# Kernel tuning notes

Measured on AMD Instinct MI355X. Metric: run time of the kernel, lower is better.

Reference implementation:

```python
import jax, jax.numpy as jnp
import numpy as np

EPS = 1e-8  # torch F.cosine_similarity default eps


def setup_inputs() -> dict:
    key = jax.random.key(0)
    k1, k2 = jax.random.split(key)
    B, D, C = 8192, 1024, 1000
    x = jax.random.normal(k1, (B, D), dtype=jnp.float32)
    W = jax.random.normal(k2, (D, C), dtype=jnp.float32) * 0.02
    b = jnp.zeros((C,), dtype=jnp.float32)
    return {"x": x, "W": W, "b": b}


def reference(x, W, b):
    B = x.shape[0]
    # classifier logits -> softmax probs
    logits = x @ W + b                              # [B, C]
    logp = jax.nn.log_softmax(logits, axis=1)       # [B, C]
    pred = jnp.exp(logp)
    # per-row sum of p * log p (negative entropy), matches pred*log(pred) loop
    loss = jnp.sum(pred * logp, axis=-1)            # [B]
    # per-row mean cosine similarity against all rows (incl. self)
    norms = jnp.maximum(jnp.linalg.norm(x, axis=1, keepdims=True), EPS)
    xn = x / norms                                  # [B, D]
    sim = xn @ xn.T                                 # [B, B]
    weight = jnp.sum(sim, axis=1) / B               # [B]
    return loss * weight
```

## Files before the change

kernel.cpp:

```cpp
#include <hip/hip_runtime.h>
#include <hip/hip_bf16.h>
#include <cstdint>
#include <cstddef>

typedef __attribute__((ext_vector_type(8))) short bf16x8;
typedef __attribute__((ext_vector_type(4))) float f32x4;

__device__ __forceinline__ unsigned short f2bf(float f) {
  union { float f; unsigned u; } v; v.f = f;
  unsigned r = v.u + 0x7FFFu + ((v.u >> 16) & 1u);
  return (unsigned short)(r >> 16);
}

__device__ __forceinline__ float bf2f(unsigned short h) {
  union { float f; unsigned u; } c; c.u = ((unsigned)h) << 16;
  return c.f;
}

__device__ __forceinline__ void gload_lds16(const void* g, void* l) {
  __builtin_amdgcn_global_load_lds(
      (const __attribute__((address_space(1))) unsigned int*)g,
      (__attribute__((address_space(3))) unsigned int*)l, 16, 0, 0);
}

__global__ __launch_bounds__(1024) void k01_prep(const float* __restrict__ W,
                                                 unsigned short* __restrict__ wtf,
                                                 const float* __restrict__ x,
                                                 unsigned short* __restrict__ xbf,
                                                 float* __restrict__ rnorm,
                                                 float* __restrict__ sp) {
  __shared__ __align__(16) char sm[83968];
  int tid = threadIdx.x;
  int b = blockIdx.x;
  int lane = tid & 63;
  int wid = tid >> 6;

  int k0 = (b & 15) * 64;
  int c0 = (b >> 4) * 64;
  int tx = tid & 63;
  int ty = tid >> 6;
  float wreg[4];
#pragma unroll
  for (int i = 0; i < 4; ++i) {
    int c = c0 + tx;
    wreg[i] = (c < 1000) ? W[(size_t)(k0 + i * 16 + ty) * 1000 + c] : 0.f;
  }

  {
    float (*sblk)[1024] = (float(*)[1024])sm;
    int row0 = b * 32 + wid * 2;
    const float4* xr0 = (const float4*)(x + (size_t)row0 * 1024);
    const float4* xr1 = (const float4*)(x + (size_t)(row0 + 1) * 1024);
    float4 v[2][4];
#pragma unroll
    for (int j = 0; j < 4; ++j) v[0][j] = xr0[lane + j * 64];
#pragma unroll
    for (int j = 0; j < 4; ++j) v[1][j] = xr1[lane + j * 64];
    float ss0 = 0.f, ss1 = 0.f;
#pragma unroll
    for (int j = 0; j < 4; ++j) {
      ss0 += v[0][j].x * v[0][j].x + v[0][j].y * v[0][j].y +
             v[0][j].z * v[0][j].z + v[0][j].w * v[0][j].w;
      ss1 += v[1][j].x * v[1][j].x + v[1][j].y * v[1][j].y +
             v[1][j].z * v[1][j].z + v[1][j].w * v[1][j].w;
    }
#pragma unroll
    for (int m = 1; m < 64; m <<= 1) {
      ss0 += __shfl_xor(ss0, m);
      ss1 += __shfl_xor(ss1, m);
    }
    float rn0 = 1.f / fmaxf(sqrtf(ss0), 1e-8f);
    float rn1 = 1.f / fmaxf(sqrtf(ss1), 1e-8f);
    if (lane == 0) {
      rnorm[row0] = rn0;
      rnorm[row0 + 1] = rn1;
    }
    float4 sacc[4];
#pragma unroll
    for (int j = 0; j < 4; ++j) {
      ushort4 h0, h1;
      h0.x = f2bf(v[0][j].x); h0.y = f2bf(v[0][j].y);
      h0.z = f2bf(v[0][j].z); h0.w = f2bf(v[0][j].w);
      h1.x = f2bf(v[1][j].x); h1.y = f2bf(v[1][j].y);
      h1.z = f2bf(v[1][j].z); h1.w = f2bf(v[1][j].w);
      ((ushort4*)(xbf + (size_t)row0 * 1024))[lane + j * 64] = h0;
      ((ushort4*)(xbf + (size_t)(row0 + 1) * 1024))[lane + j * 64] = h1;
      sacc[j].x = v[0][j].x * rn0 + v[1][j].x * rn1;
      sacc[j].y = v[0][j].y * rn0 + v[1][j].y * rn1;
      sacc[j].z = v[0][j].z * rn0 + v[1][j].z * rn1;
      sacc[j].w = v[0][j].w * rn0 + v[1][j].w * rn1;
    }
#pragma unroll
    for (int j = 0; j < 4; ++j) ((float4*)sblk[wid])[j * 64 + lane] = sacc[j];
    __syncthreads();
    float acc = 0.f;
#pragma unroll
    for (int w = 0; w < 16; ++w) acc += sblk[w][tid];
    sp[(size_t)b * 1024 + tid] = acc;
  }

  {
    float (*tile2)[72] = (float(*)[72])(sm + 65536);
#pragma unroll
    for (int i = 0; i < 4; ++i) tile2[tx][i * 16 + ty] = wreg[i];
    __syncthreads();
    if (tid < 512) {
      int fi = tid >> 6;
      int l = tid & 63;
      int cf = fi >> 1;
      int kf = fi & 1;
      int r2 = cf * 16 + (l & 15);
      int c2 = kf * 32 + (l >> 4) * 8;
      float4 va = *(const float4*)&tile2[r2][c2];
      float4 vb = *(const float4*)&tile2[r2][c2 + 4];
      uint4 o;
      o.x = (unsigned)f2bf(va.x) | ((unsigned)f2bf(va.y) << 16);
      o.y = (unsigned)f2bf(va.z) | ((unsigned)f2bf(va.w) << 16);
      o.z = (unsigned)f2bf(vb.x) | ((unsigned)f2bf(vb.y) << 16);
      o.w = (unsigned)f2bf(vb.z) | ((unsigned)f2bf(vb.w) << 16);
      size_t fg = (size_t)(c0 / 16 + cf) * 32 + (k0 / 32 + kf);
      *(uint4*)((char*)wtf + fg * 1024 + (size_t)l * 16) = o;
    }
  }
}

__global__ __launch_bounds__(256) void k2_sred(const float* __restrict__ sp,
                                               float* __restrict__ s) {
  __shared__ float red[4][64];
  int t = threadIdx.x;
  int dd = t & 63;
  int g = t >> 6;
  int d = blockIdx.x * 64 + dd;
  float acc = 0.f;
#pragma unroll 8
  for (int b = g * 64; b < g * 64 + 64; ++b) acc += sp[(size_t)b * 1024 + d];
  red[g][dd] = acc;
  __syncthreads();
  if (g == 0) s[d] = red[0][dd] + red[1][dd] + red[2][dd] + red[3][dd];
}

__global__ __launch_bounds__(256) void k3_gemm(const unsigned short* __restrict__ xbf,
                                               const unsigned short* __restrict__ wtf,
                                               const float* __restrict__ bias,
                                               float* __restrict__ pm,
                                               float* __restrict__ pz,
                                               float* __restrict__ ps) {
  __shared__ __align__(16) char lds[32768];

  int tid = threadIdx.x;
  int lane = tid & 63;
  int wid = tid >> 6;
  int wc = wid & 1;
  int wr = wid >> 1;
  int cb = blockIdx.x >> 6;
  int rb = blockIdx.x & 63;
  int C0 = cb * 128;
  int R0 = rb * 128;

  float bv[4][4];
#pragma unroll
  for (int mf = 0; mf < 4; ++mf)
#pragma unroll
    for (int q = 0; q < 4; ++q) {
      int cls_g = C0 + wc * 64 + mf * 16 + (lane >> 4) * 4 + q;
      bv[mf][q] = (cls_g < 1000) ? bias[cls_g] : -1e30f;
    }
  f32x4 acc[4][4];
#pragma unroll
  for (int mf = 0; mf < 4; ++mf)
#pragma unroll
    for (int nf = 0; nf < 4; ++nf)
#pragma unroll
      for (int q = 0; q < 4; ++q) acc[mf][nf][q] = bv[mf][q];

  const char* gB = (const char*)(xbf + (size_t)R0 * 1024);
  int grow = (tid >> 3) & 7;
  int gswz = ((tid & 7) ^ grow) << 4;

  auto stageB = [&](int kt, int bb) {
    char* lB = lds + bb * 16384;
#pragma unroll
    for (int i = 0; i < 4; ++i) {
      size_t row = i * 32 + (tid >> 3);
      gload_lds16(gB + row * 2048 + kt * 128 + gswz, lB + i * 4096 + tid * 16);
    }
  };

  const char* gAf = (const char*)wtf +
                    ((size_t)(cb * 8 + wc * 4) * 32) * 1024 + (size_t)lane * 16;

  int rsw = (lane & 7) << 4;
  int kcol = (lane >> 4) * 16;

  stageB(0, 0);
  __syncthreads();
  int cur = 0;
  for (int t = 0; t < 16; ++t) {
    if (t < 15) stageB(t + 1, cur ^ 1);
    bf16x8 a[4][2], bb[4][2];
#pragma unroll
    for (int mf = 0; mf < 4; ++mf)
#pragma unroll
      for (int ks = 0; ks < 2; ++ks)
        a[mf][ks] = *(const bf16x8*)(gAf + (size_t)(mf * 32 + t * 2 + ks) * 1024);
    const char* B = lds + cur * 16384;
#pragma unroll
    for (int nf = 0; nf < 4; ++nf)
#pragma unroll
      for (int ks = 0; ks < 2; ++ks)
        bb[nf][ks] = *(const bf16x8*)(B + (wr * 64 + nf * 16 + (lane & 15)) * 128 +
                                      ((ks * 64 + kcol) ^ rsw));
    __builtin_amdgcn_s_setprio(1);
#pragma unroll
    for (int ks = 0; ks < 2; ++ks)
#pragma unroll
      for (int mf = 0; mf < 4; ++mf)
#pragma unroll
        for (int nf = 0; nf < 4; ++nf)
          acc[mf][nf] = __builtin_amdgcn_mfma_f32_16x16x32_bf16(a[mf][ks], bb[nf][ks],
                                                                acc[mf][nf], 0, 0, 0);
    __builtin_amdgcn_s_setprio(0);
    __syncthreads();
    cur ^= 1;
  }

  float* mm = (float*)lds;
  float* zz = mm + 256;
  float* sv = zz + 256;
#pragma unroll
  for (int nf = 0; nf < 4; ++nf) {
    float m1 = -1e30f;
#pragma unroll
    for (int mf = 0; mf < 4; ++mf)
#pragma unroll
      for (int q = 0; q < 4; ++q) m1 = fmaxf(m1, acc[mf][nf][q]);
    m1 = fmaxf(m1, __shfl_xor(m1, 16));
    m1 = fmaxf(m1, __shfl_xor(m1, 32));
    float z1 = 0.f, s1 = 0.f;
#pragma unroll
    for (int mf = 0; mf < 4; ++mf)
#pragma unroll
      for (int q = 0; q < 4; ++q) {
        float tt = acc[mf][nf][q] - m1;
        float e = expf(tt);
        z1 += e;
        s1 += e * tt;
      }
    z1 += __shfl_xor(z1, 16); z1 += __shfl_xor(z1, 32);
    s1 += __shfl_xor(s1, 16); s1 += __shfl_xor(s1, 32);
    if (lane < 16) {
      int r = wr * 64 + nf * 16 + lane;
      mm[wc * 128 + r] = m1;
      zz[wc * 128 + r] = z1;
      sv[wc * 128 + r] = s1;
    }
  }
  __syncthreads();
  if (tid < 128) {
    float m0 = mm[tid], mA = mm[128 + tid];
    float z0 = zz[tid], zA = zz[128 + tid];
    float s0 = sv[tid], sA = sv[128 + tid];
    float M = fmaxf(m0, mA);
    float e0 = expf(m0 - M), e1 = expf(mA - M);
    float Z = z0 * e0 + zA * e1;
    float S = e0 * (s0 + (m0 - M) * z0) + e1 * (sA + (mA - M) * zA);
    size_t o = (size_t)cb * 8192 + R0 + tid;
    pm[o] = M;
    pz[o] = Z;
    ps[o] = S;
  }
}

__global__ __launch_bounds__(256) void k4_final(const unsigned short* __restrict__ xbf,
                                                const float* __restrict__ s,
                                                const float* __restrict__ rnorm,
                                                const float* __restrict__ pm,
                                                const float* __restrict__ pz,
                                                const float* __restrict__ ps,
                                                float* __restrict__ out) {
  int tid = threadIdx.x;
  int wid = tid >> 6, lane = tid & 63;
  int row = blockIdx.x * 4 + wid;
  const bf16x8* xr = (const bf16x8*)(xbf + (size_t)row * 1024);
  const float4* s4 = (const float4*)s;
  float dot = 0.f;
#pragma unroll
  for (int j = 0; j < 2; ++j) {
    bf16x8 v = xr[lane + j * 64];
    float4 sa = s4[(lane + j * 64) * 2];
    float4 sb = s4[(lane + j * 64) * 2 + 1];
    dot += bf2f((unsigned short)v[0]) * sa.x + bf2f((unsigned short)v[1]) * sa.y +
           bf2f((unsigned short)v[2]) * sa.z + bf2f((unsigned short)v[3]) * sa.w +
           bf2f((unsigned short)v[4]) * sb.x + bf2f((unsigned short)v[5]) * sb.y +
           bf2f((unsigned short)v[6]) * sb.z + bf2f((unsigned short)v[7]) * sb.w;
  }
#pragma unroll
  for (int m = 1; m < 64; m <<= 1) dot += __shfl_xor(dot, m);
  if (lane == 0) {
    float mv[8], zv[8], svv[8];
    float M = -1e30f;
#pragma unroll
    for (int c = 0; c < 8; ++c) {
      mv[c] = pm[(size_t)c * 8192 + row];
      zv[c] = pz[(size_t)c * 8192 + row];
      svv[c] = ps[(size_t)c * 8192 + row];
      M = fmaxf(M, mv[c]);
    }
    float Z = 0.f, S = 0.f;
#pragma unroll
    for (int c = 0; c < 8; ++c) {
      float e = expf(mv[c] - M);
      Z += zv[c] * e;
      S += e * (svv[c] + (mv[c] - M) * zv[c]);
    }
    float loss = S / Z - logf(Z);
    out[row] = loss * dot * rnorm[row] * (1.f / 8192.f);
  }
}

extern "C" void kernel_launch(void* const* d_in, const int* in_sizes, int n_in,
                              void* d_out, int out_size, void* d_ws, size_t ws_size,
                              hipStream_t stream) {
  (void)in_sizes; (void)n_in; (void)out_size; (void)ws_size;
  const float* x = (const float*)d_in[0];
  const float* W = (const float*)d_in[1];
  const float* b = (const float*)d_in[2];
  float* out = (float*)d_out;
  char* ws = (char*)d_ws;

  unsigned short* wtf = (unsigned short*)(ws + 0);
  unsigned short* xbf = (unsigned short*)(ws + 2097152);
  float* rnorm = (float*)(ws + 18874368);
  float* s = (float*)(ws + 18907136);
  float* sp = (float*)(ws + 18915328);
  float* pm = (float*)(ws + 18915328);
  float* pz = (float*)(ws + 18915328 + 262144);
  float* ps = (float*)(ws + 18915328 + 524288);

  k01_prep<<<256, 1024, 0, stream>>>(W, wtf, x, xbf, rnorm, sp);
  k2_sred<<<16, 256, 0, stream>>>(sp, s);
  k3_gemm<<<512, 256, 0, stream>>>(xbf, wtf, b, pm, pz, ps);
  k4_final<<<2048, 256, 0, stream>>>(xbf, s, rnorm, pm, pz, ps, out);
}
```

Baseline: 54.14 us.

## Fold cosine dot into GEMM padding column and deepen B pipeline

The column-sum vector s is written as bf16 into the unused padded class column 1000 of the packed W tile, so the GEMM produces x·s as an extra logit. That value is pulled out and masked before the softmax reduction, which removes the separate per-row dot pass over xbf in the final kernel. The GEMM also grows to 256-row tiles with 512 threads and a 4-buffer, 128KB LDS ring with explicit vmcnt waits, and the A fragments are double-buffered in registers. The cost is lower occupancy and fragile hand-written waitcnt scheduling, plus bf16 rounding of s.

Measured after the change: 47.19 us. -12.8%, faster.

```diff
diff --git a/kernel.cpp b/kernel.cpp
--- a/kernel.cpp
+++ b/kernel.cpp
@@ -125,7 +125,8 @@
 }
 
 __global__ __launch_bounds__(256) void k2_sred(const float* __restrict__ sp,
-                                               float* __restrict__ s) {
+                                               float* __restrict__ s,
+                                               unsigned short* __restrict__ wtf) {
   __shared__ float red[4][64];
   int t = threadIdx.x;
   int dd = t & 63;
@@ -136,26 +137,34 @@
   for (int b = g * 64; b < g * 64 + 64; ++b) acc += sp[(size_t)b * 1024 + d];
   red[g][dd] = acc;
   __syncthreads();
-  if (g == 0) s[d] = red[0][dd] + red[1][dd] + red[2][dd] + red[3][dd];
-}
-
-__global__ __launch_bounds__(256) void k3_gemm(const unsigned short* __restrict__ xbf,
+  if (g == 0) {
+    float sv = red[0][dd] + red[1][dd] + red[2][dd] + red[3][dd];
+    s[d] = sv;
+    int kf = d >> 5;
+    int j = d & 31;
+    int l = ((j >> 3) << 4) | 8;
+    wtf[((size_t)62 * 32 + kf) * 512 + (size_t)l * 8 + (j & 7)] = f2bf(sv);
+  }
+}
+
+__global__ __launch_bounds__(512) void k3_gemm(const unsigned short* __restrict__ xbf,
                                                const unsigned short* __restrict__ wtf,
                                                const float* __restrict__ bias,
                                                float* __restrict__ pm,
                                                float* __restrict__ pz,
-                                               float* __restrict__ ps) {
-  __shared__ __align__(16) char lds[32768];
+                                               float* __restrict__ ps,
+                                               float* __restrict__ pd) {
+  __shared__ __align__(16) char lds[131072];
 
   int tid = threadIdx.x;
   int lane = tid & 63;
   int wid = tid >> 6;
   int wc = wid & 1;
   int wr = wid >> 1;
-  int cb = blockIdx.x >> 6;
-  int rb = blockIdx.x & 63;
+  int cb = blockIdx.x >> 5;
+  int rb = blockIdx.x & 31;
   int C0 = cb * 128;
-  int R0 = rb * 128;
+  int R0 = rb * 256;
 
   float bv[4][4];
 #pragma unroll
@@ -163,7 +172,7 @@
 #pragma unroll
     for (int q = 0; q < 4; ++q) {
       int cls_g = C0 + wc * 64 + mf * 16 + (lane >> 4) * 4 + q;
-      bv[mf][q] = (cls_g < 1000) ? bias[cls_g] : -1e30f;
+      bv[mf][q] = (cls_g < 1000) ? bias[cls_g] : ((cls_g == 1000) ? 0.f : -1e30f);
     }
   f32x4 acc[4][4];
 #pragma unroll
@@ -174,42 +183,37 @@
       for (int q = 0; q < 4; ++q) acc[mf][nf][q] = bv[mf][q];
 
   const char* gB = (const char*)(xbf + (size_t)R0 * 1024);
-  int grow = (tid >> 3) & 7;
-  int gswz = ((tid & 7) ^ grow) << 4;
-
-  auto stageB = [&](int kt, int bb) {
-    char* lB = lds + bb * 16384;
-#pragma unroll
-    for (int i = 0; i < 4; ++i) {
-      size_t row = i * 32 + (tid >> 3);
-      gload_lds16(gB + row * 2048 + kt * 128 + gswz, lB + i * 4096 + tid * 16);
+  int gswz = ((tid & 7) ^ ((tid >> 3) & 7)) << 4;
+
+  auto stageB = [&](int kt, char* lB) {
+#pragma unroll
+    for (int r = 0; r < 4; ++r) {
+      size_t row = r * 64 + (tid >> 3);
+      gload_lds16(gB + row * 2048 + kt * 128 + gswz, lB + r * 8192 + wid * 1024);
     }
   };
 
   const char* gAf = (const char*)wtf +
                     ((size_t)(cb * 8 + wc * 4) * 32) * 1024 + (size_t)lane * 16;
+  bf16x8 aA[4][2], aB[4][2];
+  auto loadA = [&](bf16x8(&dst)[4][2], int t) {
+#pragma unroll
+    for (int mf = 0; mf < 4; ++mf)
+#pragma unroll
+      for (int ks = 0; ks < 2; ++ks)
+        dst[mf][ks] = *(const bf16x8*)(gAf + (size_t)(mf * 32 + t * 2 + ks) * 1024);
+  };
 
   int rsw = (lane & 7) << 4;
   int kcol = (lane >> 4) * 16;
-
-  stageB(0, 0);
-  __syncthreads();
-  int cur = 0;
-  for (int t = 0; t < 16; ++t) {
-    if (t < 15) stageB(t + 1, cur ^ 1);
-    bf16x8 a[4][2], bb[4][2];
-#pragma unroll
-    for (int mf = 0; mf < 4; ++mf)
+  auto comp = [&](const char* B, bf16x8(&a)[4][2]) {
+    bf16x8 bbf[4][2];
+#pragma unroll
+    for (int nf = 0; nf < 4; ++nf)
 #pragma unroll
       for (int ks = 0; ks < 2; ++ks)
-        a[mf][ks] = *(const bf16x8*)(gAf + (size_t)(mf * 32 + t * 2 + ks) * 1024);
-    const char* B = lds + cur * 16384;
-#pragma unroll
-    for (int nf = 0; nf < 4; ++nf)
-#pragma unroll
-      for (int ks = 0; ks < 2; ++ks)
-        bb[nf][ks] = *(const bf16x8*)(B + (wr * 64 + nf * 16 + (lane & 15)) * 128 +
-                                      ((ks * 64 + kcol) ^ rsw));
+        bbf[nf][ks] = *(const bf16x8*)(B + (wr * 64 + nf * 16 + (lane & 15)) * 128 +
+                                       ((ks * 64 + kcol) ^ rsw));
     __builtin_amdgcn_s_setprio(1);
 #pragma unroll
     for (int ks = 0; ks < 2; ++ks)
@@ -217,16 +221,66 @@
       for (int mf = 0; mf < 4; ++mf)
 #pragma unroll
         for (int nf = 0; nf < 4; ++nf)
-          acc[mf][nf] = __builtin_amdgcn_mfma_f32_16x16x32_bf16(a[mf][ks], bb[nf][ks],
+          acc[mf][nf] = __builtin_amdgcn_mfma_f32_16x16x32_bf16(a[mf][ks], bbf[nf][ks],
                                                                 acc[mf][nf], 0, 0, 0);
     __builtin_amdgcn_s_setprio(0);
-    __syncthreads();
-    cur ^= 1;
-  }
-
+  };
+
+#define WAIT12 asm volatile("s_waitcnt vmcnt(12)" ::: "memory"); \
+  __builtin_amdgcn_s_barrier(); asm volatile("" ::: "memory")
+
+  stageB(0, lds);
+  loadA(aA, 0);
+  stageB(1, lds + 32768);
+
+  for (int tt = 0; tt < 12; tt += 4) {
+    loadA(aB, tt + 1);
+    WAIT12;
+    stageB(tt + 2, lds + 2 * 32768);
+    comp(lds, aA);
+    loadA(aA, tt + 2);
+    WAIT12;
+    stageB(tt + 3, lds + 3 * 32768);
+    comp(lds + 32768, aB);
+    loadA(aB, tt + 3);
+    WAIT12;
+    stageB(tt + 4, lds);
+    comp(lds + 2 * 32768, aA);
+    loadA(aA, tt + 4);
+    WAIT12;
+    stageB(tt + 5, lds + 32768);
+    comp(lds + 3 * 32768, aB);
+  }
+  loadA(aB, 13);
+  WAIT12;
+  stageB(14, lds + 2 * 32768);
+  comp(lds, aA);
+  loadA(aA, 14);
+  WAIT12;
+  stageB(15, lds + 3 * 32768);
+  comp(lds + 32768, aB);
+  loadA(aB, 15);
+  WAIT12;
+  comp(lds + 2 * 32768, aA);
+  asm volatile("s_waitcnt vmcnt(0)" ::: "memory");
+  __builtin_amdgcn_s_barrier();
+  asm volatile("" ::: "memory");
+  comp(lds + 3 * 32768, aB);
+#undef WAIT12
+
+  if (cb == 7 && wc == 1 && ((lane >> 4) == 2)) {
+#pragma unroll
+    for (int nf = 0; nf < 4; ++nf) {
+      int r = wr * 64 + nf * 16 + (lane & 15);
+      pd[(size_t)rb * 256 + r] = acc[2][nf][0];
+      acc[2][nf][0] = -1e30f;
+    }
+  }
+
+  __syncthreads();
   float* mm = (float*)lds;
-  float* zz = mm + 256;
-  float* sv = zz + 256;
+  float* zz = mm + 512;
+  float* sv = zz + 512;
 #pragma unroll
   for (int nf = 0; nf < 4; ++nf) {
     float m1 = -1e30f;
@@ -241,25 +295,25 @@
     for (int mf = 0; mf < 4; ++mf)
 #pragma unroll
       for (int q = 0; q < 4; ++q) {
-        float tt = acc[mf][nf][q] - m1;
-        float e = expf(tt);
+        float tt2 = acc[mf][nf][q] - m1;
+        float e = expf(tt2);
         z1 += e;
-        s1 += e * tt;
+        s1 += e * tt2;
       }
     z1 += __shfl_xor(z1, 16); z1 += __shfl_xor(z1, 32);
     s1 += __shfl_xor(s1, 16); s1 += __shfl_xor(s1, 32);
     if (lane < 16) {
       int r = wr * 64 + nf * 16 + lane;
-      mm[wc * 128 + r] = m1;
-      zz[wc * 128 + r] = z1;
-      sv[wc * 128 + r] = s1;
+      mm[wc * 256 + r] = m1;
+      zz[wc * 256 + r] = z1;
+      sv[wc * 256 + r] = s1;
     }
   }
   __syncthreads();
-  if (tid < 128) {
-    float m0 = mm[tid], mA = mm[128 + tid];
-    float z0 = zz[tid], zA = zz[128 + tid];
-    float s0 = sv[tid], sA = sv[128 + tid];
+  if (tid < 256) {
+    float m0 = mm[tid], mA = mm[256 + tid];
+    float z0 = zz[tid], zA = zz[256 + tid];
+    float s0 = sv[tid], sA = sv[256 + tid];
     float M = fmaxf(m0, mA);
     float e0 = expf(m0 - M), e1 = expf(mA - M);
     float Z = z0 * e0 + zA * e1;
@@ -271,51 +325,31 @@
   }
 }
 
-__global__ __launch_bounds__(256) void k4_final(const unsigned short* __restrict__ xbf,
-                                                const float* __restrict__ s,
-                                                const float* __restrict__ rnorm,
+__global__ __launch_bounds__(256) void k4_final(const float* __restrict__ rnorm,
                                                 const float* __restrict__ pm,
                                                 const float* __restrict__ pz,
                                                 const float* __restrict__ ps,
+                                                const float* __restrict__ pd,
                                                 float* __restrict__ out) {
-  int tid = threadIdx.x;
-  int wid = tid >> 6, lane = tid & 63;
-  int row = blockIdx.x * 4 + wid;
-  const bf16x8* xr = (const bf16x8*)(xbf + (size_t)row * 1024);
-  const float4* s4 = (const float4*)s;
-  float dot = 0.f;
-#pragma unroll
-  for (int j = 0; j < 2; ++j) {
-    bf16x8 v = xr[lane + j * 64];
-    float4 sa = s4[(lane + j * 64) * 2];
-    float4 sb = s4[(lane + j * 64) * 2 + 1];
-    dot += bf2f((unsigned short)v[0]) * sa.x + bf2f((unsigned short)v[1]) * sa.y +
-           bf2f((unsigned short)v[2]) * sa.z + bf2f((unsigned short)v[3]) * sa.w +
-           bf2f((unsigned short)v[4]) * sb.x + bf2f((unsigned short)v[5]) * sb.y +
-           bf2f((unsigned short)v[6]) * sb.z + bf2f((unsigned short)v[7]) * sb.w;
-  }
-#pragma unroll
-  for (int m = 1; m < 64; m <<= 1) dot += __shfl_xor(dot, m);
-  if (lane == 0) {
-    float mv[8], zv[8], svv[8];
-    float M = -1e30f;
-#pragma unroll
-    for (int c = 0; c < 8; ++c) {
-      mv[c] = pm[(size_t)c * 8192 + row];
-      zv[c] = pz[(size_t)c * 8192 + row];
-      svv[c] = ps[(size_t)c * 8192 + row];
-      M = fmaxf(M, mv[c]);
-    }
-    float Z = 0.f, S = 0.f;
-#pragma unroll
-    for (int c = 0; c < 8; ++c) {
-      float e = expf(mv[c] - M);
-      Z += zv[c] * e;
-      S += e * (svv[c] + (mv[c] - M) * zv[c]);
-    }
-    float loss = S / Z - logf(Z);
-    out[row] = loss * dot * rnorm[row] * (1.f / 8192.f);
-  }
+  int row = blockIdx.x * 256 + threadIdx.x;
+  float mv[8], zv[8], svv[8];
+  float M = -1e30f;
+#pragma unroll
+  for (int c = 0; c < 8; ++c) {
+    mv[c] = pm[(size_t)c * 8192 + row];
+    zv[c] = pz[(size_t)c * 8192 + row];
+    svv[c] = ps[(size_t)c * 8192 + row];
+    M = fmaxf(M, mv[c]);
+  }
+  float Z = 0.f, S = 0.f;
+#pragma unroll
+  for (int c = 0; c < 8; ++c) {
+    float e = expf(mv[c] - M);
+    Z += zv[c] * e;
+    S += e * (svv[c] + (mv[c] - M) * zv[c]);
+  }
+  float loss = S / Z - logf(Z);
+  out[row] = loss * pd[row] * rnorm[row] * (1.f / 8192.f);
 }
 
 extern "C" void kernel_launch(void* const* d_in, const int* in_sizes, int n_in,
@@ -336,9 +370,10 @@
   float* pm = (float*)(ws + 18915328);
   float* pz = (float*)(ws + 18915328 + 262144);
   float* ps = (float*)(ws + 18915328 + 524288);
+  float* pd = (float*)(ws + 18915328 + 786432);
 
   k01_prep<<<256, 1024, 0, stream>>>(W, wtf, x, xbf, rnorm, sp);
-  k2_sred<<<16, 256, 0, stream>>>(sp, s);
-  k3_gemm<<<512, 256, 0, stream>>>(xbf, wtf, b, pm, pz, ps);
-  k4_final<<<2048, 256, 0, stream>>>(xbf, s, rnorm, pm, pz, ps, out);
-}
+  k2_sred<<<16, 256, 0, stream>>>(sp, s, wtf);
+  k3_gemm<<<256, 512, 0, stream>>>(xbf, wtf, b, pm, pz, ps, pd);
+  k4_final<<<32, 256, 0, stream>>>(rnorm, pm, pz, ps, pd, out);
+}
```
